# Optimization experiments

Measured on AMD Instinct MI355X. Metric: run time of the kernel, lower is better.

## Reference

```python
import jax, jax.numpy as jnp
import numpy as np
from jax import lax

EPSILON = 100.0
NITER = 10
ERR_TOL = 0.1


def setup_inputs() -> dict:
    key = jax.random.key(0)
    k1, k2 = jax.random.split(key)
    n, d = 2048, 64
    return {
        "output": jax.random.normal(k1, (n, d), dtype=jnp.float32),
        "target": jax.random.normal(k2, (n, d), dtype=jnp.float32),
    }


def reference(output, target):
    n = output.shape[0]
    eps = jnp.float32(EPSILON)
    # NOTE: despite the name, the original computes L1 (sum of abs) pairwise distances.
    C = jnp.sum(jnp.abs(output[:, None, :] - target[None, :, :]), axis=-1)  # [n, n]
    log_mu = jnp.log(jnp.full((n,), 1.0 / n, dtype=jnp.float32))  # mu == nu == 1/n

    def M(u, v):
        return (-C + u[:, None] + v[None, :]) / eps

    def lse(A):  # matches original: log(sum(exp(A), axis=1) + 1e-6), not max-stabilized
        return jnp.log(jnp.exp(A).sum(axis=1) + 1e-6)

    def step(carry, _):
        u, v, done = carry
        u_new = eps * (log_mu - lse(M(u, v))) + u
        v_new = eps * (log_mu - lse(M(u_new, v).T)) + v
        err = jnp.abs(u_new - u).sum()
        # original applies this iteration's update, then breaks if err < tol
        u = jnp.where(done, u, u_new)
        v = jnp.where(done, v, v_new)
        done = done | (err < ERR_TOL)
        return (u, v, done), None

    u0 = jnp.zeros((n,), dtype=jnp.float32)
    v0 = jnp.zeros((n,), dtype=jnp.float32)
    (u, v, _), _ = lax.scan(step, (u0, v0, jnp.array(False)), None, length=NITER)

    Gamma = jnp.exp(M(u, v))
    return jnp.sum(Gamma * C)
```

## Files before the change

kernel.cpp:

```cpp
#include <hip/hip_runtime.h>


#define N 2048
#define EPS 100.0f
#define INV_EPS 0.01f
#define LOG_MU (-7.6246189861593985f)
#define MU (4.8828125e-4f)
#define NITER 10
#define TOL 0.1f

typedef _Float16 h16x8 __attribute__((ext_vector_type(8)));
typedef _Float16 h16x4 __attribute__((ext_vector_type(4)));

__device__ __forceinline__ float wave_sum(float s) {
  #pragma unroll
  for (int off = 32; off > 0; off >>= 1) s += __shfl_down(s, off, 64);
  return s;
}

__global__ __launch_bounds__(256) void build_k(const float* __restrict__ A,
                                               const float* __restrict__ B,
                                               _Float16* __restrict__ K,
                                               _Float16* __restrict__ KT,
                                               float* __restrict__ z_hist,
                                               float* __restrict__ w_hist,
                                               float* __restrict__ u_hist,
                                               int* __restrict__ idx_arr,
                                               int* __restrict__ done_arr) {
  __shared__ float As[64][68];
  __shared__ float Bs[64][68];
  __shared__ float T[64][68];
  const int b = blockIdx.x;
  const int g = b & 7, t = b >> 3;
  const int itl = t >> 5, jt = t & 31;
  const int i0 = (g * 4 + itl) * 64, j0 = jt * 64;
  const int tid = threadIdx.x;
  if (b == 0) {
    #pragma unroll
    for (int q = 0; q < 8; ++q) {
      int r = q * 256 + tid;
      z_hist[r] = 1.f; w_hist[r] = 1.f; u_hist[r] = 0.f;
    }
    if (tid == 0) { idx_arr[0] = 0; done_arr[0] = 0; }
  }
  #pragma unroll
  for (int e = 0; e < 16; ++e) {
    int idx = e * 256 + tid;
    int r = idx >> 6, k = idx & 63;
    As[k][r] = A[(i0 + r) * 64 + k];
    Bs[k][r] = B[(j0 + r) * 64 + k];
  }
  __syncthreads();
  const int ty = tid >> 4, tx = tid & 15;
  float acc[4][4] = {};
  #pragma unroll 8
  for (int k = 0; k < 64; ++k) {
    float4 av = *(const float4*)&As[k][ty * 4];
    float4 bv = *(const float4*)&Bs[k][tx * 4];
    float a[4] = {av.x, av.y, av.z, av.w};
    float c[4] = {bv.x, bv.y, bv.z, bv.w};
    #pragma unroll
    for (int p = 0; p < 4; ++p)
      #pragma unroll
      for (int q = 0; q < 4; ++q)
        acc[p][q] += fabsf(a[p] - c[q]);
  }
  #pragma unroll
  for (int p = 0; p < 4; ++p) {
    float4 e4 = make_float4(expf(-acc[p][0] * INV_EPS), expf(-acc[p][1] * INV_EPS),
                            expf(-acc[p][2] * INV_EPS), expf(-acc[p][3] * INV_EPS));
    h16x4 kv;
    kv[0] = (_Float16)e4.x; kv[1] = (_Float16)e4.y;
    kv[2] = (_Float16)e4.z; kv[3] = (_Float16)e4.w;
    *(h16x4*)&K[(size_t)(i0 + ty * 4 + p) * N + j0 + tx * 4] = kv;
    T[ty * 4 + p][tx * 4 + 0] = e4.x;
    T[ty * 4 + p][tx * 4 + 1] = e4.y;
    T[ty * 4 + p][tx * 4 + 2] = e4.z;
    T[ty * 4 + p][tx * 4 + 3] = e4.w;
  }
  __syncthreads();
  #pragma unroll
  for (int p = 0; p < 4; ++p) {
    int jl = ty * 4 + p;
    h16x4 o;
    o[0] = (_Float16)T[tx * 4 + 0][jl]; o[1] = (_Float16)T[tx * 4 + 1][jl];
    o[2] = (_Float16)T[tx * 4 + 2][jl]; o[3] = (_Float16)T[tx * 4 + 3][jl];
    *(h16x4*)&KT[(size_t)(j0 + jl) * N + i0 + tx * 4] = o;
  }
}

__global__ __launch_bounds__(256) void rowz(const _Float16* __restrict__ K,
    float* __restrict__ z_hist, const float* __restrict__ w_hist,
    float* __restrict__ u_hist, const int* __restrict__ idx_arr,
    const int* __restrict__ done_arr, int it) {
  if (done_arr[it]) return;
  __shared__ float wl[N];
  const int tid = threadIdx.x, wv = tid >> 6, lane = tid & 63;
  const int b = blockIdx.x;
  const int rbase = ((b & 7) << 8) + ((b >> 3) << 2);
  const int idx = idx_arr[it];
  {
    const float* __restrict__ wc = w_hist + (size_t)idx * N;
    *(float4*)&wl[tid * 8]     = *(const float4*)(wc + tid * 8);
    *(float4*)&wl[tid * 8 + 4] = *(const float4*)(wc + tid * 8 + 4);
  }
  __syncthreads();
  const int r = rbase + wv;
  const _Float16* __restrict__ Krow = K + (size_t)r * N;
  float s = 0.f;
  #pragma unroll
  for (int p = 0; p < 4; ++p) {
    int j = lane * 8 + p * 512;
    h16x8 k8 = *(const h16x8*)(Krow + j);
    float4 wa = *(const float4*)&wl[j];
    float4 wb = *(const float4*)&wl[j + 4];
    s += (float)k8[0] * wa.x + (float)k8[1] * wa.y
       + (float)k8[2] * wa.z + (float)k8[3] * wa.w
       + (float)k8[4] * wb.x + (float)k8[5] * wb.y
       + (float)k8[6] * wb.z + (float)k8[7] * wb.w;
  }
  s = wave_sum(s);
  if (lane == 0) {
    float zc = z_hist[(size_t)idx * N + r];
    float den = zc * s + 1e-6f;
    z_hist[(size_t)(it + 1) * N + r] = zc * MU / den;
    u_hist[(size_t)(it + 1) * N + r] =
        EPS * (LOG_MU - logf(den)) + u_hist[(size_t)idx * N + r];
  }
}

__global__ __launch_bounds__(256) void colw(const _Float16* __restrict__ KT,
    const float* __restrict__ z_hist, float* __restrict__ w_hist,
    const float* __restrict__ u_hist, int* __restrict__ idx_arr,
    int* __restrict__ done_arr, int it) {
  const int tid = threadIdx.x, wv = tid >> 6, lane = tid & 63;
  const int b = blockIdx.x;
  const int dprev = done_arr[it];
  if (dprev) {
    if (b == 0 && tid == 0) { idx_arr[it + 1] = idx_arr[it]; done_arr[it + 1] = 1; }
    return;
  }
  __shared__ float zl[N];
  const int jbase = ((b & 7) << 8) + ((b >> 3) << 2);
  const int idx = idx_arr[it];
  {
    const float* __restrict__ zn = z_hist + (size_t)(it + 1) * N;
    *(float4*)&zl[tid * 8]     = *(const float4*)(zn + tid * 8);
    *(float4*)&zl[tid * 8 + 4] = *(const float4*)(zn + tid * 8 + 4);
  }
  __syncthreads();
  const int j = jbase + wv;
  const _Float16* __restrict__ Kc = KT + (size_t)j * N;
  float s = 0.f;
  #pragma unroll
  for (int p = 0; p < 4; ++p) {
    int i = lane * 8 + p * 512;
    h16x8 k8 = *(const h16x8*)(Kc + i);
    float4 za = *(const float4*)&zl[i];
    float4 zb = *(const float4*)&zl[i + 4];
    s += (float)k8[0] * za.x + (float)k8[1] * za.y
       + (float)k8[2] * za.z + (float)k8[3] * za.w
       + (float)k8[4] * zb.x + (float)k8[5] * zb.y
       + (float)k8[6] * zb.z + (float)k8[7] * zb.w;
  }
  s = wave_sum(s);
  if (lane == 0) {
    float wc = w_hist[(size_t)idx * N + j];
    float den = wc * s + 1e-6f;
    w_hist[(size_t)(it + 1) * N + j] = wc * MU / den;
  }
  if (b == 0) {
    const float* __restrict__ un = u_hist + (size_t)(it + 1) * N;
    const float* __restrict__ uc = u_hist + (size_t)idx * N;
    float e = 0.f;
    #pragma unroll
    for (int p = 0; p < 2; ++p) {
      int i = tid * 4 + p * 1024;
      float4 a = *(const float4*)(un + i);
      float4 c = *(const float4*)(uc + i);
      e += fabsf(a.x - c.x) + fabsf(a.y - c.y)
         + fabsf(a.z - c.z) + fabsf(a.w - c.w);
    }
    e = wave_sum(e);
    __shared__ float sh4[4];
    if (lane == 0) sh4[wv] = e;
    __syncthreads();
    if (tid == 0) {
      float err = (sh4[0] + sh4[1]) + (sh4[2] + sh4[3]);
      idx_arr[it + 1] = it + 1;
      done_arr[it + 1] = (err < TOL) ? 1 : 0;
    }
  }
}

__global__ __launch_bounds__(512) void loss_pass(const _Float16* __restrict__ K,
    const float* __restrict__ z_hist, const float* __restrict__ w_hist,
    const int* __restrict__ idx_arr, float* __restrict__ losspart) {
  __shared__ float wl[N];
  __shared__ float sh8[8];
  const int tid = threadIdx.x, wv = tid >> 6, lane = tid & 63;
  const int b = blockIdx.x;
  const int rbase = ((b & 7) << 8) + ((b >> 3) << 3);
  const int idx = idx_arr[NITER];
  *(float4*)&wl[tid * 4] = *(const float4*)(w_hist + (size_t)idx * N + tid * 4);
  __syncthreads();
  const int r = rbase + wv;
  const _Float16* __restrict__ Krow = K + (size_t)r * N;
  float s = 0.f;
  #pragma unroll
  for (int p = 0; p < 4; ++p) {
    int j = lane * 8 + p * 512;
    h16x8 k8 = *(const h16x8*)(Krow + j);
    #pragma unroll
    for (int q = 0; q < 8; ++q) {
      float kf = (float)k8[q];
      s += kf * wl[j + q] * (-EPS * logf(kf));
    }
  }
  s = wave_sum(s);
  if (lane == 0) sh8[wv] = s * z_hist[(size_t)idx * N + r];
  __syncthreads();
  if (tid == 0)
    losspart[b] = ((sh8[0] + sh8[1]) + (sh8[2] + sh8[3]))
                + ((sh8[4] + sh8[5]) + (sh8[6] + sh8[7]));
}

__global__ __launch_bounds__(256) void loss_reduce(const float* __restrict__ losspart,
                                                   float* __restrict__ out) {
  float s = losspart[threadIdx.x];
  s = wave_sum(s);
  __shared__ float sh4[4];
  if ((threadIdx.x & 63) == 0) sh4[threadIdx.x >> 6] = s;
  __syncthreads();
  if (threadIdx.x == 0) out[0] = (sh4[0] + sh4[1]) + (sh4[2] + sh4[3]);
}

extern "C" void kernel_launch(void* const* d_in, const int* in_sizes, int n_in,
                              void* d_out, int out_size, void* d_ws, size_t ws_size,
                              hipStream_t stream) {
  const float* A = (const float*)d_in[0];
  const float* B = (const float*)d_in[1];
  float* out = (float*)d_out;

  char* base = (char*)d_ws;
  _Float16* K    = (_Float16*)base;
  _Float16* KT   = (_Float16*)(base + (size_t)N * N * 2);
  float* z_hist  = (float*)(base + (size_t)2 * N * N * 2);
  float* w_hist  = z_hist + (size_t)(NITER + 1) * N;
  float* u_hist  = w_hist + (size_t)(NITER + 1) * N;
  float* losspart= u_hist + (size_t)(NITER + 1) * N;
  int*   idx_arr = (int*)(losspart + 256);
  int*   done_arr= idx_arr + (NITER + 1);

  build_k<<<1024, 256, 0, stream>>>(A, B, K, KT, z_hist, w_hist, u_hist,
                                    idx_arr, done_arr);
  for (int it = 0; it < NITER; ++it) {
    rowz<<<512, 256, 0, stream>>>(K, z_hist, w_hist, u_hist, idx_arr,
                                  done_arr, it);
    colw<<<512, 256, 0, stream>>>(KT, z_hist, w_hist, u_hist, idx_arr,
                                  done_arr, it);
  }
  loss_pass<<<256, 512, 0, stream>>>(K, z_hist, w_hist, idx_arr, losspart);
  loss_reduce<<<1, 256, 0, stream>>>(losspart, out);
}
```

Before: 73.14 us.

## Use 512-thread blocks for row/col passes, alias LDS, fast exp/log intrinsics

```diff
diff --git a/kernel.cpp b/kernel.cpp
--- a/kernel.cpp
+++ b/kernel.cpp
@@ -29,7 +29,6 @@
                                                int* __restrict__ done_arr) {
   __shared__ float As[64][68];
   __shared__ float Bs[64][68];
-  __shared__ float T[64][68];
   const int b = blockIdx.x;
   const int g = b & 7, t = b >> 3;
   const int itl = t >> 5, jt = t & 31;
@@ -65,10 +64,12 @@
       for (int q = 0; q < 4; ++q)
         acc[p][q] += fabsf(a[p] - c[q]);
   }
-  #pragma unroll
-  for (int p = 0; p < 4; ++p) {
-    float4 e4 = make_float4(expf(-acc[p][0] * INV_EPS), expf(-acc[p][1] * INV_EPS),
-                            expf(-acc[p][2] * INV_EPS), expf(-acc[p][3] * INV_EPS));
+  __syncthreads();
+  float (*T)[68] = As;
+  #pragma unroll
+  for (int p = 0; p < 4; ++p) {
+    float4 e4 = make_float4(__expf(-acc[p][0] * INV_EPS), __expf(-acc[p][1] * INV_EPS),
+                            __expf(-acc[p][2] * INV_EPS), __expf(-acc[p][3] * INV_EPS));
     h16x4 kv;
     kv[0] = (_Float16)e4.x; kv[1] = (_Float16)e4.y;
     kv[2] = (_Float16)e4.z; kv[3] = (_Float16)e4.w;
@@ -89,7 +90,7 @@
   }
 }
 
-__global__ __launch_bounds__(256) void rowz(const _Float16* __restrict__ K,
+__global__ __launch_bounds__(512) void rowz(const _Float16* __restrict__ K,
     float* __restrict__ z_hist, const float* __restrict__ w_hist,
     float* __restrict__ u_hist, const int* __restrict__ idx_arr,
     const int* __restrict__ done_arr, int it) {
@@ -97,13 +98,9 @@
   __shared__ float wl[N];
   const int tid = threadIdx.x, wv = tid >> 6, lane = tid & 63;
   const int b = blockIdx.x;
-  const int rbase = ((b & 7) << 8) + ((b >> 3) << 2);
+  const int rbase = ((b & 7) << 8) + ((b >> 3) << 3);
   const int idx = idx_arr[it];
-  {
-    const float* __restrict__ wc = w_hist + (size_t)idx * N;
-    *(float4*)&wl[tid * 8]     = *(const float4*)(wc + tid * 8);
-    *(float4*)&wl[tid * 8 + 4] = *(const float4*)(wc + tid * 8 + 4);
-  }
+  *(float4*)&wl[tid * 4] = *(const float4*)(w_hist + (size_t)idx * N + tid * 4);
   __syncthreads();
   const int r = rbase + wv;
   const _Float16* __restrict__ Krow = K + (size_t)r * N;
@@ -129,7 +126,7 @@
   }
 }
 
-__global__ __launch_bounds__(256) void colw(const _Float16* __restrict__ KT,
+__global__ __launch_bounds__(512) void colw(const _Float16* __restrict__ KT,
     const float* __restrict__ z_hist, float* __restrict__ w_hist,
     const float* __restrict__ u_hist, int* __restrict__ idx_arr,
     int* __restrict__ done_arr, int it) {
@@ -141,13 +138,9 @@
     return;
   }
   __shared__ float zl[N];
-  const int jbase = ((b & 7) << 8) + ((b >> 3) << 2);
+  const int jbase = ((b & 7) << 8) + ((b >> 3) << 3);
   const int idx = idx_arr[it];
-  {
-    const float* __restrict__ zn = z_hist + (size_t)(it + 1) * N;
-    *(float4*)&zl[tid * 8]     = *(const float4*)(zn + tid * 8);
-    *(float4*)&zl[tid * 8 + 4] = *(const float4*)(zn + tid * 8 + 4);
-  }
+  *(float4*)&zl[tid * 4] = *(const float4*)(z_hist + (size_t)(it + 1) * N + tid * 4);
   __syncthreads();
   const int j = jbase + wv;
   const _Float16* __restrict__ Kc = KT + (size_t)j * N;
@@ -172,21 +165,17 @@
   if (b == 0) {
     const float* __restrict__ un = u_hist + (size_t)(it + 1) * N;
     const float* __restrict__ uc = u_hist + (size_t)idx * N;
-    float e = 0.f;
-    #pragma unroll
-    for (int p = 0; p < 2; ++p) {
-      int i = tid * 4 + p * 1024;
-      float4 a = *(const float4*)(un + i);
-      float4 c = *(const float4*)(uc + i);
-      e += fabsf(a.x - c.x) + fabsf(a.y - c.y)
-         + fabsf(a.z - c.z) + fabsf(a.w - c.w);
-    }
+    float4 a = *(const float4*)(un + tid * 4);
+    float4 c = *(const float4*)(uc + tid * 4);
+    float e = fabsf(a.x - c.x) + fabsf(a.y - c.y)
+            + fabsf(a.z - c.z) + fabsf(a.w - c.w);
     e = wave_sum(e);
-    __shared__ float sh4[4];
-    if (lane == 0) sh4[wv] = e;
+    __shared__ float sh8[8];
+    if (lane == 0) sh8[wv] = e;
     __syncthreads();
     if (tid == 0) {
-      float err = (sh4[0] + sh4[1]) + (sh4[2] + sh4[3]);
+      float err = ((sh8[0] + sh8[1]) + (sh8[2] + sh8[3]))
+                + ((sh8[4] + sh8[5]) + (sh8[6] + sh8[7]));
       idx_arr[it + 1] = it + 1;
       done_arr[it + 1] = (err < TOL) ? 1 : 0;
     }
@@ -214,7 +203,7 @@
     #pragma unroll
     for (int q = 0; q < 8; ++q) {
       float kf = (float)k8[q];
-      s += kf * wl[j + q] * (-EPS * logf(kf));
+      s += kf * wl[j + q] * (-EPS * __logf(kf));
     }
   }
   s = wave_sum(s);
@@ -255,9 +244,9 @@
   build_k<<<1024, 256, 0, stream>>>(A, B, K, KT, z_hist, w_hist, u_hist,
                                     idx_arr, done_arr);
   for (int it = 0; it < NITER; ++it) {
-    rowz<<<512, 256, 0, stream>>>(K, z_hist, w_hist, u_hist, idx_arr,
+    rowz<<<256, 512, 0, stream>>>(K, z_hist, w_hist, u_hist, idx_arr,
                                   done_arr, it);
-    colw<<<512, 256, 0, stream>>>(KT, z_hist, w_hist, u_hist, idx_arr,
+    colw<<<256, 512, 0, stream>>>(KT, z_hist, w_hist, u_hist, idx_arr,
                                   done_arr, it);
   }
   loss_pass<<<256, 512, 0, stream>>>(K, z_hist, w_hist, idx_arr, losspart);
```

New measurement: 74.42 us. No clear change (+1.8%).
